# Kernel tuning notes

Measured on AMD Instinct MI355X. Metric: run time of the kernel, lower is better.

The kernel has to match this reference:

```python
import jax, jax.numpy as jnp
import numpy as np

B, S, D, H, DK, F = 4, 2048, 1024, 16, 64, 4096


def layer_norm(x, g, b, eps=1e-5):
    mu = jnp.mean(x, axis=-1, keepdims=True)
    var = jnp.var(x, axis=-1, keepdims=True)
    return (x - mu) * jax.lax.rsqrt(var + eps) * g + b


def setup_inputs() -> dict:
    key = jax.random.key(0)
    ks = jax.random.split(key, 16)
    s = 0.02
    return {
        "src": jax.random.normal(ks[0], (B, S, D), jnp.float32),
        # per-head q/k/v projections stacked over heads: (H, D, DK)
        "Wq": jax.random.normal(ks[1], (H, D, DK), jnp.float32) * s,
        "bq": jnp.zeros((H, DK), jnp.float32),
        "Wk": jax.random.normal(ks[2], (H, D, DK), jnp.float32) * s,
        "bk": jnp.zeros((H, DK), jnp.float32),
        "Wv": jax.random.normal(ks[3], (H, D, DK), jnp.float32) * s,
        "bv": jnp.zeros((H, DK), jnp.float32),
        "Wo": jax.random.normal(ks[4], (H * DK, D), jnp.float32) * s,
        "bo": jnp.zeros((D,), jnp.float32),
        "ln1_g": jnp.ones((D,), jnp.float32),
        "ln1_b": jnp.zeros((D,), jnp.float32),
        "W1": jax.random.normal(ks[5], (D, F), jnp.float32) * s,
        "b1": jnp.zeros((F,), jnp.float32),
        "W2": jax.random.normal(ks[6], (F, D), jnp.float32) * s,
        "b2": jnp.zeros((D,), jnp.float32),
        "ln2_g": jnp.ones((D,), jnp.float32),
        "ln2_b": jnp.zeros((D,), jnp.float32),
    }


def reference(src, Wq, bq, Wk, bk, Wv, bv, Wo, bo, ln1_g, ln1_b, W1, b1, W2, b2, ln2_g, ln2_b):
    # --- multi-head attention (all heads batched via einsum) ---
    q = jnp.einsum("bsd,hdk->bhsk", src, Wq) + bq[None, :, None, :]
    k = jnp.einsum("bsd,hdk->bhsk", src, Wk) + bk[None, :, None, :]
    v = jnp.einsum("bsd,hdk->bhsk", src, Wv) + bv[None, :, None, :]
    scale = jnp.sqrt(jnp.asarray(DK, q.dtype))
    scores = jnp.einsum("bhqk,bhsk->bhqs", q, k) / scale  # [B,H,S,S]
    p = jax.nn.softmax(scores, axis=-1)
    ctx = jnp.einsum("bhqs,bhsk->bhqk", p, v)             # [B,H,S,DK]
    ctx = ctx.transpose(0, 2, 1, 3).reshape(src.shape[0], src.shape[1], H * DK)
    attn_out = ctx @ Wo + bo
    x = layer_norm(src + attn_out, ln1_g, ln1_b)
    # --- feed-forward ---
    ff = jax.nn.relu(x @ W1 + b1) @ W2 + b2
    return layer_norm(x + ff, ln2_g, ln2_b)
```

## Files before the change

### kernel.cpp

```cpp
#include <hip/hip_runtime.h>
#include <hip/hip_bf16.h>
#include <cstddef>
#include <cstdint>

typedef __bf16 bf16;
typedef __bf16 bf16x4 __attribute__((ext_vector_type(4)));
typedef __bf16 bf16x8 __attribute__((ext_vector_type(8)));
typedef float f32x4 __attribute__((ext_vector_type(4)));

#define GLD_LDS16(g, l) __builtin_amdgcn_global_load_lds( \
    (const __attribute__((address_space(1))) void*)(g),   \
    (__attribute__((address_space(3))) void*)(l), 16, 0, 0)

__global__ void __launch_bounds__(256)
k_cast(const float* __restrict__ in, bf16* __restrict__ out) {
  int gid = blockIdx.x * 256 + threadIdx.x;
  f32x4 a = ((const f32x4*)in)[gid * 2];
  f32x4 b = ((const f32x4*)in)[gid * 2 + 1];
  bf16x8 o;
#pragma unroll
  for (int i = 0; i < 4; ++i) { o[i] = (bf16)a[i]; o[i + 4] = (bf16)b[i]; }
  ((bf16x8*)out)[gid] = o;
}

__global__ void __launch_bounds__(256)
k_transpose_t(const float* __restrict__ in, bf16* __restrict__ out, int R, int C) {
  __shared__ float tile[64][68];
  const int nct = C >> 6;
  const int bc = blockIdx.x % nct, br = blockIdx.x / nct;
  const int r0 = br << 6, c0 = bc << 6;
  const int t = threadIdx.x;
  const int tr = t >> 4, tc4 = (t & 15) << 2;
#pragma unroll
  for (int i = 0; i < 4; ++i)
    *(f32x4*)&tile[i * 16 + tr][tc4] =
        *(const f32x4*)&in[(size_t)(r0 + i * 16 + tr) * C + c0 + tc4];
  __syncthreads();
  const int c = t >> 2, rch = (t & 3) << 4;
  bf16 ob[16];
#pragma unroll
  for (int j = 0; j < 16; ++j) ob[j] = (bf16)tile[rch + j][c];
  bf16* dst = out + (size_t)(c0 + c) * R + r0 + rch;
  *(bf16x8*)&dst[0] = *(bf16x8*)&ob[0];
  *(bf16x8*)&dst[8] = *(bf16x8*)&ob[8];
}

__global__ void __launch_bounds__(256)
k_reorder_qkv_t(const float* __restrict__ Wq, const float* __restrict__ Wk,
                const float* __restrict__ Wv, bf16* __restrict__ WqkvT) {
  __shared__ float tile[64][68];
  const int bid = blockIdx.x;
  const int sub = bid >> 4, tl = bid & 15;
  const int proj = sub >> 4, h = sub & 15;
  const float* W = (proj == 0) ? Wq : (proj == 1) ? Wk : Wv;
  const float* src = W + (size_t)h * 65536;
  const int r0 = tl << 6;
  const int t = threadIdx.x, tr = t >> 4, tc4 = (t & 15) << 2;
#pragma unroll
  for (int i = 0; i < 4; ++i)
    *(f32x4*)&tile[i * 16 + tr][tc4] =
        *(const f32x4*)&src[(size_t)(r0 + i * 16 + tr) * 64 + tc4];
  __syncthreads();
  const int c = t >> 2, rch = (t & 3) << 4;
  bf16 ob[16];
#pragma unroll
  for (int j = 0; j < 16; ++j) ob[j] = (bf16)tile[rch + j][c];
  bf16* dst = WqkvT + ((size_t)(proj * 1024 + h * 64 + c)) * 1024 + r0 + rch;
  *(bf16x8*)&dst[0] = *(bf16x8*)&ob[0];
  *(bf16x8*)&dst[8] = *(bf16x8*)&ob[8];
}

__global__ void __launch_bounds__(256)
k_bias_qkv(const float* __restrict__ bq, const float* __restrict__ bk,
           const float* __restrict__ bv, float* __restrict__ bqkv) {
  int n = blockIdx.x * 256 + threadIdx.x;
  int proj = n >> 10, wi = n & 1023;
  const float* bb = (proj == 0) ? bq : (proj == 1) ? bk : bv;
  bqkv[n] = bb[wi];
}

template <int MODE>
__global__ void __launch_bounds__(256)
k_gemm_bt(const bf16* __restrict__ A, const bf16* __restrict__ Bt,
          const float* __restrict__ bias, void* __restrict__ outp,
          int M, int N, int K,
          bf16* __restrict__ qb, bf16* __restrict__ kb, bf16* __restrict__ vb) {
  __shared__ __align__(16) bf16 As[2][128][32];
  __shared__ __align__(16) bf16 Bs[2][128][32];
  const int tid = threadIdx.x;
  const int wave = tid >> 6, lane = tid & 63;
  const int l16 = lane & 15, lq = lane >> 4;
  const int mtiles = M >> 7;
  const int tile_m = (blockIdx.x % mtiles) << 7;
  const int tile_n = (blockIdx.x / mtiles) << 7;
  const int wm = (wave >> 1) << 6, wn = (wave & 1) << 6;

  const bf16* Arow = A + (size_t)tile_m * K;
  const bf16* Brow = Bt + (size_t)tile_n * K;
  bf16* As_f = &As[0][0][0];
  bf16* Bs_f = &Bs[0][0][0];

  int gA[4], rA[4], kA[4];
#pragma unroll
  for (int j = 0; j < 4; ++j) {
    gA[j] = j * 4 + wave;
    rA[j] = (gA[j] & 7) * 16 + (lane >> 2);
    kA[j] = (gA[j] >> 3) * 32 + (lane & 3) * 8;
  }

  f32x4 acc[4][4] = {};

  for (int k0 = 0; k0 < K; k0 += 64) {
    __syncthreads();
#pragma unroll
    for (int j = 0; j < 4; ++j) {
      GLD_LDS16(Arow + (size_t)rA[j] * K + k0 + kA[j], As_f + gA[j] * 512);
      GLD_LDS16(Brow + (size_t)rA[j] * K + k0 + kA[j], Bs_f + gA[j] * 512);
    }
    __syncthreads();
#pragma unroll
    for (int p = 0; p < 2; ++p) {
      bf16x8 af[4], bfr[4];
#pragma unroll
      for (int mi = 0; mi < 4; ++mi)
        af[mi] = *(const bf16x8*)&As[p][wm + mi * 16 + l16][lq * 8];
#pragma unroll
      for (int ni = 0; ni < 4; ++ni)
        bfr[ni] = *(const bf16x8*)&Bs[p][wn + ni * 16 + l16][lq * 8];
#pragma unroll
      for (int mi = 0; mi < 4; ++mi)
#pragma unroll
        for (int ni = 0; ni < 4; ++ni)
          acc[mi][ni] = __builtin_amdgcn_mfma_f32_16x16x32_bf16(af[mi], bfr[ni], acc[mi][ni], 0, 0, 0);
    }
  }

#pragma unroll
  for (int mi = 0; mi < 4; ++mi) {
#pragma unroll
    for (int ni = 0; ni < 4; ++ni) {
      const int gn = tile_n + wn + ni * 16 + l16;
      const float bb = bias[gn];
      f32x4 v = acc[mi][ni];
      const int gm0 = tile_m + wm + mi * 16 + lq * 4;
      if (MODE == 0) {
        int proj = gn >> 10, wi = gn & 1023;
        int h = wi >> 6, dk = wi & 63;
        int b = gm0 >> 11, sdx = gm0 & 2047;
        size_t bhs = (size_t)((b << 4) + h);
        if (proj == 0) {
#pragma unroll
          for (int i = 0; i < 4; ++i)
            qb[(bhs * 2048 + sdx + i) * 64 + dk] = (bf16)((v[i] + bb) * 0.18033688f);
        } else if (proj == 1) {
#pragma unroll
          for (int i = 0; i < 4; ++i)
            kb[(bhs * 2048 + sdx + i) * 64 + dk] = (bf16)(v[i] + bb);
        } else {
          bf16x4 pk;
#pragma unroll
          for (int i = 0; i < 4; ++i) pk[i] = (bf16)(v[i] + bb);
          *(bf16x4*)&vb[(bhs * 64 + dk) * 2048 + sdx] = pk;
        }
      } else if (MODE == 1) {
#pragma unroll
        for (int i = 0; i < 4; ++i)
          ((bf16*)outp)[(size_t)(gm0 + i) * N + gn] = (bf16)(v[i] + bb);
      } else {
#pragma unroll
        for (int i = 0; i < 4; ++i)
          ((bf16*)outp)[(size_t)(gm0 + i) * N + gn] = (bf16)fmaxf(v[i] + bb, 0.f);
      }
    }
  }
}

__global__ void __launch_bounds__(256)
k_attn(const bf16* __restrict__ qb, const bf16* __restrict__ kb,
       const bf16* __restrict__ vb, bf16* __restrict__ ctx) {
  __shared__ __align__(16) bf16 Ks[128][72];
  __shared__ __align__(16) bf16 Vs[64][136];
  __shared__ __align__(16) bf16 Ps[4][16][136];

  const int bid = blockIdx.x;
  const int qt = bid & 15, bh = bid >> 4;
  const bf16* Q  = qb + (size_t)bh * 131072 + (size_t)qt * 8192;
  const bf16* Kp = kb + (size_t)bh * 131072;
  const bf16* Vp = vb + (size_t)bh * 131072;

  const int tid = threadIdx.x, wave = tid >> 6, lane = tid & 63;
  const int l16 = lane & 15, lq = lane >> 4;

  const bf16* qrowA = Q + (size_t)(wave * 32 + l16) * 64;
  const bf16* qrowB = qrowA + 16 * 64;
  const bf16x8 qA0 = *(const bf16x8*)(qrowA + lq * 8);
  const bf16x8 qA1 = *(const bf16x8*)(qrowA + 32 + lq * 8);
  const bf16x8 qB0 = *(const bf16x8*)(qrowB + lq * 8);
  const bf16x8 qB1 = *(const bf16x8*)(qrowB + 32 + lq * 8);

  bf16* Pw = &Ps[wave][0][0];

  float lA = 0.f, lB = 0.f;
  f32x4 oA[4] = {}, oB[4] = {};

  for (int kt = 0; kt < 16; ++kt) {
    const int s0 = kt << 7;
    __syncthreads();
#pragma unroll
    for (int c = 0; c < 4; ++c) {
      int cc = tid + c * 256;
      *(bf16x8*)&Ks[cc >> 3][(cc & 7) * 8] =
          *(const bf16x8*)&Kp[(size_t)s0 * 64 + cc * 8];
    }
#pragma unroll
    for (int c = 0; c < 4; ++c) {
      int cc = tid + c * 256;
      *(bf16x8*)&Vs[cc >> 4][(cc & 15) * 8] =
          *(const bf16x8*)&Vp[(size_t)(cc >> 4) * 2048 + s0 + (cc & 15) * 8];
    }
    __syncthreads();

    f32x4 zA[8], zB[8];
#pragma unroll
    for (int ni = 0; ni < 8; ++ni) {
      bf16x8 b0 = *(const bf16x8*)&Ks[ni * 16 + l16][lq * 8];
      bf16x8 b1 = *(const bf16x8*)&Ks[ni * 16 + l16][32 + lq * 8];
      f32x4 z = {};
      z = __builtin_amdgcn_mfma_f32_16x16x32_bf16(b0, qA0, z, 0, 0, 0);
      zA[ni] = __builtin_amdgcn_mfma_f32_16x16x32_bf16(b1, qA1, z, 0, 0, 0);
      f32x4 w = {};
      w = __builtin_amdgcn_mfma_f32_16x16x32_bf16(b0, qB0, w, 0, 0, 0);
      zB[ni] = __builtin_amdgcn_mfma_f32_16x16x32_bf16(b1, qB1, w, 0, 0, 0);
    }

    bf16x8 paA[4], paB[4];
#pragma unroll
    for (int ni = 0; ni < 8; ++ni) {
      bf16x4 pk;
#pragma unroll
      for (int i = 0; i < 4; ++i) {
        float pe = exp2f(zA[ni][i]);
        lA += pe;
        pk[i] = (bf16)pe;
      }
      *(bf16x4*)&Pw[l16 * 136 + ni * 16 + lq * 4] = pk;
    }
#pragma unroll
    for (int ks = 0; ks < 4; ++ks)
      paA[ks] = *(const bf16x8*)&Pw[l16 * 136 + ks * 32 + lq * 8];

#pragma unroll
    for (int ni = 0; ni < 8; ++ni) {
      bf16x4 pk;
#pragma unroll
      for (int i = 0; i < 4; ++i) {
        float pe = exp2f(zB[ni][i]);
        lB += pe;
        pk[i] = (bf16)pe;
      }
      *(bf16x4*)&Pw[l16 * 136 + ni * 16 + lq * 4] = pk;
    }
#pragma unroll
    for (int ks = 0; ks < 4; ++ks)
      paB[ks] = *(const bf16x8*)&Pw[l16 * 136 + ks * 32 + lq * 8];

#pragma unroll
    for (int nd = 0; nd < 4; ++nd)
#pragma unroll
      for (int ks = 0; ks < 4; ++ks) {
        bf16x8 vf = *(const bf16x8*)&Vs[nd * 16 + l16][ks * 32 + lq * 8];
        oA[nd] = __builtin_amdgcn_mfma_f32_16x16x32_bf16(paA[ks], vf, oA[nd], 0, 0, 0);
        oB[nd] = __builtin_amdgcn_mfma_f32_16x16x32_bf16(paB[ks], vf, oB[nd], 0, 0, 0);
      }
  }

  lA += __shfl_xor(lA, 16); lA += __shfl_xor(lA, 32);
  lB += __shfl_xor(lB, 16); lB += __shfl_xor(lB, 32);
  float* lw = (float*)Pw;
  lw[l16] = lA;
  lw[16 + l16] = lB;
  float ivA[4], ivB[4];
#pragma unroll
  for (int i = 0; i < 4; ++i) {
    ivA[i] = 1.f / lw[lq * 4 + i];
    ivB[i] = 1.f / lw[16 + lq * 4 + i];
  }

  const int b = bh >> 4, h = bh & 15;
  const int row0 = qt * 128 + wave * 32 + lq * 4;
#pragma unroll
  for (int i = 0; i < 4; ++i) {
#pragma unroll
    for (int nd = 0; nd < 4; ++nd) {
      int dk = nd * 16 + l16;
      ctx[((size_t)(b * 2048 + row0 + i)) * 1024 + h * 64 + dk] = (bf16)(oA[nd][i] * ivA[i]);
      ctx[((size_t)(b * 2048 + row0 + 16 + i)) * 1024 + h * 64 + dk] = (bf16)(oB[nd][i] * ivB[i]);
    }
  }
}

template <typename RT, typename DT, typename OT>
__global__ void __launch_bounds__(256)
k_ln(const RT* __restrict__ resid, const DT* __restrict__ delta,
     const float* __restrict__ g, const float* __restrict__ bta,
     OT* __restrict__ out) {
  const int row = blockIdx.x, tid = threadIdx.x;
  const int wave = tid >> 6, lane = tid & 63;
  __shared__ float rs_[4], rs2_[4];
  const RT* r = resid + (size_t)row * 1024;
  const DT* d = delta + (size_t)row * 1024;
  OT* o = out + (size_t)row * 1024;
  float x[4], s = 0.f, s2 = 0.f;
#pragma unroll
  for (int j = 0; j < 4; ++j) {
    int idx = tid + j * 256;
    float v = (float)r[idx] + (float)d[idx];
    x[j] = v; s += v; s2 += v * v;
  }
#pragma unroll
  for (int m = 32; m >= 1; m >>= 1) { s += __shfl_xor(s, m); s2 += __shfl_xor(s2, m); }
  if (lane == 0) { rs_[wave] = s; rs2_[wave] = s2; }
  __syncthreads();
  float ts = rs_[0] + rs_[1] + rs_[2] + rs_[3];
  float ts2 = rs2_[0] + rs2_[1] + rs2_[2] + rs2_[3];
  float mean = ts * (1.f / 1024.f);
  float var = ts2 * (1.f / 1024.f) - mean * mean;
  float rstd = rsqrtf(var + 1e-5f);
#pragma unroll
  for (int j = 0; j < 4; ++j) {
    int idx = tid + j * 256;
    o[idx] = (OT)((x[j] - mean) * rstd * g[idx] + bta[idx]);
  }
}

extern "C" void kernel_launch(void* const* d_in, const int* in_sizes, int n_in,
                              void* d_out, int out_size, void* d_ws, size_t ws_size,
                              hipStream_t stream) {
  const float* src  = (const float*)d_in[0];
  const float* Wq   = (const float*)d_in[1];
  const float* bq   = (const float*)d_in[2];
  const float* Wk   = (const float*)d_in[3];
  const float* bk   = (const float*)d_in[4];
  const float* Wv   = (const float*)d_in[5];
  const float* bv   = (const float*)d_in[6];
  const float* Wo   = (const float*)d_in[7];
  const float* bo   = (const float*)d_in[8];
  const float* ln1g = (const float*)d_in[9];
  const float* ln1b = (const float*)d_in[10];
  const float* W1   = (const float*)d_in[11];
  const float* b1   = (const float*)d_in[12];
  const float* W2   = (const float*)d_in[13];
  const float* b2   = (const float*)d_in[14];
  const float* ln2g = (const float*)d_in[15];
  const float* ln2b = (const float*)d_in[16];

  char* p = (char*)d_ws;
  bf16*  WqkvT = (bf16*)p;  p += (size_t)3072 * 1024 * 2;
  float* bqkv  = (float*)p; p += 16384;
  bf16*  WoT   = (bf16*)p;  p += (size_t)1024 * 1024 * 2;
  bf16*  W1T   = (bf16*)p;  p += (size_t)4096 * 1024 * 2;
  bf16*  W2T   = (bf16*)p;  p += (size_t)1024 * 4096 * 2;
  bf16*  srcb  = (bf16*)p;  p += (size_t)8388608 * 2;
  bf16*  qbuf  = (bf16*)p;  p += (size_t)8388608 * 2;
  bf16*  kbuf  = (bf16*)p;  p += (size_t)8388608 * 2;
  bf16*  vbuf  = (bf16*)p;  p += (size_t)8388608 * 2;
  bf16*  ctx   = (bf16*)p;  p += (size_t)8388608 * 2;
  bf16*  x1    = (bf16*)p;  p += (size_t)8388608 * 2;
  bf16*  ff1   = (bf16*)p;  p += (size_t)8192 * 4096 * 2;
  bf16*  tmp   = qbuf;

  k_cast<<<4096, 256, 0, stream>>>(src, srcb);
  k_reorder_qkv_t<<<768, 256, 0, stream>>>(Wq, Wk, Wv, WqkvT);
  k_bias_qkv<<<12, 256, 0, stream>>>(bq, bk, bv, bqkv);
  k_transpose_t<<<256, 256, 0, stream>>>(Wo, WoT, 1024, 1024);
  k_transpose_t<<<1024, 256, 0, stream>>>(W1, W1T, 1024, 4096);
  k_transpose_t<<<1024, 256, 0, stream>>>(W2, W2T, 4096, 1024);

  k_gemm_bt<0><<<64 * 24, 256, 0, stream>>>(srcb, WqkvT, bqkv, nullptr,
                                            8192, 3072, 1024, qbuf, kbuf, vbuf);
  k_attn<<<1024, 256, 0, stream>>>(qbuf, kbuf, vbuf, ctx);
  k_gemm_bt<1><<<64 * 8, 256, 0, stream>>>(ctx, WoT, bo, tmp,
                                           8192, 1024, 1024, nullptr, nullptr, nullptr);
  k_ln<float, bf16, bf16><<<8192, 256, 0, stream>>>(src, tmp, ln1g, ln1b, x1);
  k_gemm_bt<2><<<64 * 32, 256, 0, stream>>>(x1, W1T, b1, ff1,
                                            8192, 4096, 1024, nullptr, nullptr, nullptr);
  k_gemm_bt<1><<<64 * 8, 256, 0, stream>>>(ff1, W2T, b2, tmp,
                                           8192, 1024, 4096, nullptr, nullptr, nullptr);
  k_ln<bf16, bf16, float><<<8192, 256, 0, stream>>>(x1, tmp, ln2g, ln2b, (float*)d_out);
}
```

Before: 583.6 us.

## Rewrite attention with 32x32 MFMA, register-resident P and double-buffered async KV loads

The attention kernel moves from 16x16x32 to 32x32x16 MFMA tiles, with each block covering 256 query rows over 64-key tiles. P stays in registers via packed bf16 conversion and permlane32 swaps, so the LDS round-trip for P is gone. K/V tiles are staged with global_load_lds into a swizzled, double-buffered LDS layout so the next tile loads while the current one computes. The change also adds s_setprio around MFMA sections, remaps blocks for locality, and halves the grid with a two-blocks-per-CU launch bound. It risks register pressure from the f32x16 accumulators and relies on the inline asm and swizzle layout being correct.

```diff
diff --git a/kernel.cpp b/kernel.cpp
--- a/kernel.cpp
+++ b/kernel.cpp
@@ -7,10 +7,21 @@
 typedef __bf16 bf16x4 __attribute__((ext_vector_type(4)));
 typedef __bf16 bf16x8 __attribute__((ext_vector_type(8)));
 typedef float f32x4 __attribute__((ext_vector_type(4)));
+typedef float f32x16 __attribute__((ext_vector_type(16)));
+typedef unsigned int u32x4 __attribute__((ext_vector_type(4)));
 
 #define GLD_LDS16(g, l) __builtin_amdgcn_global_load_lds( \
     (const __attribute__((address_space(1))) void*)(g),   \
     (__attribute__((address_space(3))) void*)(l), 16, 0, 0)
+
+static __device__ inline unsigned int cvtpk(float lo, float hi) {
+  unsigned int r;
+  asm("v_cvt_pk_bf16_f32 %0, %1, %2" : "=v"(r) : "v"(lo), "v"(hi));
+  return r;
+}
+static __device__ inline void plswap(unsigned int& a, unsigned int& b) {
+  asm("v_permlane32_swap_b32 %0, %1" : "+v"(a), "+v"(b));
+}
 
 __global__ void __launch_bounds__(256)
 k_cast(const float* __restrict__ in, bf16* __restrict__ out) {
@@ -175,126 +186,138 @@
   }
 }
 
-__global__ void __launch_bounds__(256)
+__global__ void __launch_bounds__(256, 2)
 k_attn(const bf16* __restrict__ qb, const bf16* __restrict__ kb,
        const bf16* __restrict__ vb, bf16* __restrict__ ctx) {
-  __shared__ __align__(16) bf16 Ks[128][72];
-  __shared__ __align__(16) bf16 Vs[64][136];
-  __shared__ __align__(16) bf16 Ps[4][16][136];
+  __shared__ __align__(16) bf16 KsL[2][4096];
+  __shared__ __align__(16) bf16 VsL[2][4096];
 
   const int bid = blockIdx.x;
-  const int qt = bid & 15, bh = bid >> 4;
-  const bf16* Q  = qb + (size_t)bh * 131072 + (size_t)qt * 8192;
-  const bf16* Kp = kb + (size_t)bh * 131072;
-  const bf16* Vp = vb + (size_t)bh * 131072;
+  const int wg = (bid & 7) * 64 + (bid >> 3);
+  const int bh = wg >> 3, qt = wg & 7;
+
+  const bf16* Qp  = qb + (size_t)bh * 131072 + (size_t)qt * 16384;
+  const bf16* Kbh = kb + (size_t)bh * 131072;
+  const bf16* Vbh = vb + (size_t)bh * 131072;
 
   const int tid = threadIdx.x, wave = tid >> 6, lane = tid & 63;
-  const int l16 = lane & 15, lq = lane >> 4;
-
-  const bf16* qrowA = Q + (size_t)(wave * 32 + l16) * 64;
-  const bf16* qrowB = qrowA + 16 * 64;
-  const bf16x8 qA0 = *(const bf16x8*)(qrowA + lq * 8);
-  const bf16x8 qA1 = *(const bf16x8*)(qrowA + 32 + lq * 8);
-  const bf16x8 qB0 = *(const bf16x8*)(qrowB + lq * 8);
-  const bf16x8 qB1 = *(const bf16x8*)(qrowB + 32 + lq * 8);
-
-  bf16* Pw = &Ps[wave][0][0];
-
+  const int l31 = lane & 31, hi = lane >> 5;
+
+  bf16x8 qfA[4], qfB[4];
+  {
+    const bf16* qra = Qp + (size_t)(wave * 64 + l31) * 64 + hi * 8;
+    const bf16* qrb = qra + 32 * 64;
+#pragma unroll
+    for (int kd = 0; kd < 4; ++kd) {
+      qfA[kd] = *(const bf16x8*)(qra + kd * 16);
+      qfB[kd] = *(const bf16x8*)(qrb + kd * 16);
+    }
+  }
+
+  const int c0 = tid, c1 = tid + 256;
+  const int sw0 = ((c0 ^ (c0 >> 3)) & 7) * 8, rw0 = c0 >> 3;
+  const int sw1 = ((c1 ^ (c1 >> 3)) & 7) * 8, rw1 = c1 >> 3;
+  const int kof0 = rw0 * 64 + sw0, kof1 = rw1 * 64 + sw1;
+  const int vof0 = rw0 * 2048 + sw0, vof1 = rw1 * 2048 + sw1;
+
+  const int xr = (hi << 4) ^ ((l31 & 7) << 4);
+  const int rb = l31 * 128 + xr;
+
+  f32x16 oA[2] = {}, oB[2] = {};
   float lA = 0.f, lB = 0.f;
-  f32x4 oA[4] = {}, oB[4] = {};
-
-  for (int kt = 0; kt < 16; ++kt) {
-    const int s0 = kt << 7;
+
+#define STAGE_KV(buf, s0)                                             \
+  do {                                                                \
+    GLD_LDS16(Kbh + (size_t)(s0) * 64 + kof0, &KsL[buf][c0 * 8]);     \
+    GLD_LDS16(Kbh + (size_t)(s0) * 64 + kof1, &KsL[buf][c1 * 8]);     \
+    GLD_LDS16(Vbh + (s0) + vof0, &VsL[buf][c0 * 8]);                  \
+    GLD_LDS16(Vbh + (s0) + vof1, &VsL[buf][c1 * 8]);                  \
+  } while (0)
+
+  STAGE_KV(0, 0);
+  __syncthreads();
+
+  for (int kt = 0; kt < 32; ++kt) {
+    const int cur = kt & 1;
+    if (kt < 31) STAGE_KV(cur ^ 1, (kt + 1) * 64);
+
+    const char* Kc = (const char*)&KsL[cur][0];
+    const char* Vc = (const char*)&VsL[cur][0];
+
+    bf16x8 paA[4], paB[4];
+#pragma unroll
+    for (int st = 0; st < 2; ++st) {
+      f32x16 sA = {}, sB = {};
+      __builtin_amdgcn_s_setprio(1);
+#pragma unroll
+      for (int kd = 0; kd < 4; ++kd) {
+        bf16x8 a = *(const bf16x8*)(Kc + st * 4096 + (rb ^ (kd << 5)));
+        sA = __builtin_amdgcn_mfma_f32_32x32x16_bf16(a, qfA[kd], sA, 0, 0, 0);
+        sB = __builtin_amdgcn_mfma_f32_32x32x16_bf16(a, qfB[kd], sB, 0, 0, 0);
+      }
+      __builtin_amdgcn_s_setprio(0);
+
+      float eA[16], eB[16];
+#pragma unroll
+      for (int i = 0; i < 16; ++i) {
+        eA[i] = exp2f(sA[i]); lA += eA[i];
+        eB[i] = exp2f(sB[i]); lB += eB[i];
+      }
+      unsigned int qdA[4][2], qdB[4][2];
+#pragma unroll
+      for (int g = 0; g < 4; ++g)
+#pragma unroll
+        for (int w = 0; w < 2; ++w) {
+          qdA[g][w] = cvtpk(eA[g * 4 + w * 2], eA[g * 4 + w * 2 + 1]);
+          qdB[g][w] = cvtpk(eB[g * 4 + w * 2], eB[g * 4 + w * 2 + 1]);
+        }
+#pragma unroll
+      for (int a2 = 0; a2 < 2; ++a2) {
+        unsigned int x0 = qdA[2 * a2][0], y0 = qdA[2 * a2 + 1][0];
+        unsigned int x1 = qdA[2 * a2][1], y1 = qdA[2 * a2 + 1][1];
+        plswap(x0, y0); plswap(x1, y1);
+        u32x4 fA = {x0, x1, y0, y1};
+        paA[st * 2 + a2] = __builtin_bit_cast(bf16x8, fA);
+        unsigned int u0 = qdB[2 * a2][0], v0 = qdB[2 * a2 + 1][0];
+        unsigned int u1 = qdB[2 * a2][1], v1 = qdB[2 * a2 + 1][1];
+        plswap(u0, v0); plswap(u1, v1);
+        u32x4 fB = {u0, u1, v0, v1};
+        paB[st * 2 + a2] = __builtin_bit_cast(bf16x8, fB);
+      }
+    }
+
+    __builtin_amdgcn_s_setprio(1);
+#pragma unroll
+    for (int nd = 0; nd < 2; ++nd)
+#pragma unroll
+      for (int ks = 0; ks < 4; ++ks) {
+        bf16x8 vf = *(const bf16x8*)(Vc + nd * 4096 + (rb ^ (ks << 5)));
+        oA[nd] = __builtin_amdgcn_mfma_f32_32x32x16_bf16(paA[ks], vf, oA[nd], 0, 0, 0);
+        oB[nd] = __builtin_amdgcn_mfma_f32_32x32x16_bf16(paB[ks], vf, oB[nd], 0, 0, 0);
+      }
+    __builtin_amdgcn_s_setprio(0);
+
     __syncthreads();
-#pragma unroll
-    for (int c = 0; c < 4; ++c) {
-      int cc = tid + c * 256;
-      *(bf16x8*)&Ks[cc >> 3][(cc & 7) * 8] =
-          *(const bf16x8*)&Kp[(size_t)s0 * 64 + cc * 8];
-    }
-#pragma unroll
-    for (int c = 0; c < 4; ++c) {
-      int cc = tid + c * 256;
-      *(bf16x8*)&Vs[cc >> 4][(cc & 15) * 8] =
-          *(const bf16x8*)&Vp[(size_t)(cc >> 4) * 2048 + s0 + (cc & 15) * 8];
-    }
-    __syncthreads();
-
-    f32x4 zA[8], zB[8];
-#pragma unroll
-    for (int ni = 0; ni < 8; ++ni) {
-      bf16x8 b0 = *(const bf16x8*)&Ks[ni * 16 + l16][lq * 8];
-      bf16x8 b1 = *(const bf16x8*)&Ks[ni * 16 + l16][32 + lq * 8];
-      f32x4 z = {};
-      z = __builtin_amdgcn_mfma_f32_16x16x32_bf16(b0, qA0, z, 0, 0, 0);
-      zA[ni] = __builtin_amdgcn_mfma_f32_16x16x32_bf16(b1, qA1, z, 0, 0, 0);
-      f32x4 w = {};
-      w = __builtin_amdgcn_mfma_f32_16x16x32_bf16(b0, qB0, w, 0, 0, 0);
-      zB[ni] = __builtin_amdgcn_mfma_f32_16x16x32_bf16(b1, qB1, w, 0, 0, 0);
-    }
-
-    bf16x8 paA[4], paB[4];
-#pragma unroll
-    for (int ni = 0; ni < 8; ++ni) {
-      bf16x4 pk;
-#pragma unroll
-      for (int i = 0; i < 4; ++i) {
-        float pe = exp2f(zA[ni][i]);
-        lA += pe;
-        pk[i] = (bf16)pe;
-      }
-      *(bf16x4*)&Pw[l16 * 136 + ni * 16 + lq * 4] = pk;
-    }
-#pragma unroll
-    for (int ks = 0; ks < 4; ++ks)
-      paA[ks] = *(const bf16x8*)&Pw[l16 * 136 + ks * 32 + lq * 8];
-
-#pragma unroll
-    for (int ni = 0; ni < 8; ++ni) {
-      bf16x4 pk;
-#pragma unroll
-      for (int i = 0; i < 4; ++i) {
-        float pe = exp2f(zB[ni][i]);
-        lB += pe;
-        pk[i] = (bf16)pe;
-      }
-      *(bf16x4*)&Pw[l16 * 136 + ni * 16 + lq * 4] = pk;
-    }
-#pragma unroll
-    for (int ks = 0; ks < 4; ++ks)
-      paB[ks] = *(const bf16x8*)&Pw[l16 * 136 + ks * 32 + lq * 8];
-
-#pragma unroll
-    for (int nd = 0; nd < 4; ++nd)
-#pragma unroll
-      for (int ks = 0; ks < 4; ++ks) {
-        bf16x8 vf = *(const bf16x8*)&Vs[nd * 16 + l16][ks * 32 + lq * 8];
-        oA[nd] = __builtin_amdgcn_mfma_f32_16x16x32_bf16(paA[ks], vf, oA[nd], 0, 0, 0);
-        oB[nd] = __builtin_amdgcn_mfma_f32_16x16x32_bf16(paB[ks], vf, oB[nd], 0, 0, 0);
-      }
-  }
-
-  lA += __shfl_xor(lA, 16); lA += __shfl_xor(lA, 32);
-  lB += __shfl_xor(lB, 16); lB += __shfl_xor(lB, 32);
-  float* lw = (float*)Pw;
-  lw[l16] = lA;
-  lw[16 + l16] = lB;
-  float ivA[4], ivB[4];
-#pragma unroll
-  for (int i = 0; i < 4; ++i) {
-    ivA[i] = 1.f / lw[lq * 4 + i];
-    ivB[i] = 1.f / lw[16 + lq * 4 + i];
-  }
+  }
+#undef STAGE_KV
+
+  const float ltA = lA + __shfl_xor(lA, 32);
+  const float ltB = lB + __shfl_xor(lB, 32);
+  const float ivA = 1.f / ltA;
+  const float ivB = 1.f / ltB;
 
   const int b = bh >> 4, h = bh & 15;
-  const int row0 = qt * 128 + wave * 32 + lq * 4;
-#pragma unroll
-  for (int i = 0; i < 4; ++i) {
-#pragma unroll
-    for (int nd = 0; nd < 4; ++nd) {
-      int dk = nd * 16 + l16;
-      ctx[((size_t)(b * 2048 + row0 + i)) * 1024 + h * 64 + dk] = (bf16)(oA[nd][i] * ivA[i]);
-      ctx[((size_t)(b * 2048 + row0 + 16 + i)) * 1024 + h * 64 + dk] = (bf16)(oB[nd][i] * ivB[i]);
+  const size_t rowbase = (size_t)(b * 2048 + qt * 256 + wave * 64);
+#pragma unroll
+  for (int r = 0; r < 16; ++r) {
+    const int qr = (r & 3) + 8 * (r >> 2) + 4 * hi;
+    const float dA = __shfl(ivA, qr);
+    const float dB = __shfl(ivB, qr);
+#pragma unroll
+    for (int nd = 0; nd < 2; ++nd) {
+      const int dk = nd * 32 + l31;
+      ctx[(rowbase + qr) * 1024 + h * 64 + dk]      = (bf16)(oA[nd][r] * dA);
+      ctx[(rowbase + 32 + qr) * 1024 + h * 64 + dk] = (bf16)(oB[nd][r] * dB);
     }
   }
 }
@@ -378,7 +401,7 @@
 
   k_gemm_bt<0><<<64 * 24, 256, 0, stream>>>(srcb, WqkvT, bqkv, nullptr,
                                             8192, 3072, 1024, qbuf, kbuf, vbuf);
-  k_attn<<<1024, 256, 0, stream>>>(qbuf, kbuf, vbuf, ctx);
+  k_attn<<<512, 256, 0, stream>>>(qbuf, kbuf, vbuf, ctx);
   k_gemm_bt<1><<<64 * 8, 256, 0, stream>>>(ctx, WoT, bo, tmp,
                                            8192, 1024, 1024, nullptr, nullptr, nullptr);
   k_ln<float, bf16, bf16><<<8192, 256, 0, stream>>>(src, tmp, ln1g, ln1b, x1);
```

New measurement: 526.9 us. 1.11x faster.
